# Kernel tuning notes

Hardware: AMD Instinct MI355X
Metric: run time of the kernel (lower is better)

## Reference

```python
import jax, jax.numpy as jnp
import numpy as np

B, S, D, H = 2, 2048, 1024, 16
HD = D // H  # head dim = 64


def setup_inputs() -> dict:
    key = jax.random.key(0)
    ks = jax.random.split(key, 5)
    scale = 1.0 / np.sqrt(D)
    return {
        "hidden_states": jax.random.normal(ks[0], (B, S, D), jnp.float32),
        "attention_mask": jax.random.normal(ks[1], (B, 1, 1, S), jnp.float32),
        "Wq": jax.random.normal(ks[2], (D, D), jnp.float32) * scale,
        "bq": jnp.zeros((D,), jnp.float32),
        "Wk": jax.random.normal(ks[3], (D, D), jnp.float32) * scale,
        "bk": jnp.zeros((D,), jnp.float32),
        "Wv": jax.random.normal(ks[4], (D, D), jnp.float32) * scale,
        "bv": jnp.zeros((D,), jnp.float32),
    }


def _split_heads(x):
    # [B,S,D] -> [B,H,S,HD]
    return x.reshape(B, S, H, HD).transpose(0, 2, 1, 3)


def reference(hidden_states, attention_mask, Wq, bq, Wk, bk, Wv, bv):
    # torch Linear: y = x @ W.T + b
    q = _split_heads(hidden_states @ Wq.T + bq)
    k = _split_heads(hidden_states @ Wk.T + bk)
    v = _split_heads(hidden_states @ Wv.T + bv)

    scores = jnp.einsum("bhqd,bhkd->bhqk", q, k)
    # Faithful to source: with a mask present, the 1/sqrt(head_dim) scaling
    # is overwritten and raw scores are multiplied by the binary key mask.
    mask = (attention_mask >= 0).astype(scores.dtype)  # [B,1,1,S]
    probs = scores * mask
    # dropout prob = 0 (eval) -> identity

    ctx = jnp.einsum("bhqk,bhkd->bhqd", probs, v)
    ctx = ctx.transpose(0, 2, 1, 3).reshape(B, S, D)
    return ctx
```

## Files before the change

### kernel.cpp

```cpp
#include <hip/hip_runtime.h>

#define BB 2
#define SS 2048
#define DD 1024
#define HH 16
#define HDIM 64
#define MTOT 4096

typedef unsigned short u16;
typedef __bf16 bf16_t;
typedef bf16_t bf16x8 __attribute__((ext_vector_type(8)));
typedef float floatx4 __attribute__((ext_vector_type(4)));
typedef float floatx16 __attribute__((ext_vector_type(16)));

__device__ __forceinline__ float bf2f(u16 u) {
  union { unsigned int i; float f; } x;
  x.i = ((unsigned int)u) << 16;
  return x.f;
}
__device__ __forceinline__ u16 f2bf(float f) {
  union { float f; unsigned int i; } x;
  x.f = f;
  unsigned int r = x.i + 0x7fffu + ((x.i >> 16) & 1u);
  return (u16)(r >> 16);
}

__device__ __forceinline__ void gload16(const u16* g, u16* l) {
  __builtin_amdgcn_global_load_lds(
      (const __attribute__((address_space(1))) unsigned int*)g,
      (__attribute__((address_space(3))) unsigned int*)l, 16, 0, 0);
}

__global__ __launch_bounds__(256) void cast_panel(
    const float* __restrict__ hs, const float* __restrict__ wq,
    const float* __restrict__ wk, const float* __restrict__ wv,
    u16* __restrict__ hs_p, u16* __restrict__ wq_p,
    u16* __restrict__ wk_p, u16* __restrict__ wv_p) {
  __shared__ u16 sT[64 * 72];
  const int bx = blockIdx.x, y = blockIdx.y;
  const float* src; u16* dst; int r0, R;
  if (bx < 64) { src = hs; dst = hs_p; r0 = bx * 64; R = 4096; }
  else {
    int w = (bx - 64) >> 4, t = (bx - 64) & 15;
    src = (w == 0) ? wq : (w == 1) ? wk : wv;
    dst = (w == 0) ? wq_p : (w == 1) ? wk_p : wv_p;
    r0 = t * 64; R = 1024;
  }
  const int c0 = y * 64;
  const int tid = threadIdx.x;
#pragma unroll
  for (int i = 0; i < 4; ++i) {
    int e = i * 256 + tid;
    int row = e >> 4, c4 = e & 15;
    float4 v = reinterpret_cast<const float4*>(src)[(size_t)(r0 + row) * 256 + (c0 >> 2) + c4];
    ushort4 o;
    o.x = f2bf(v.x); o.y = f2bf(v.y); o.z = f2bf(v.z); o.w = f2bf(v.w);
    *reinterpret_cast<ushort4*>(&sT[row * 72 + c4 * 4]) = o;
  }
  __syncthreads();
#pragma unroll
  for (int i = 0; i < 2; ++i) {
    int e = i * 256 + tid;
    int p = e >> 6, m = e & 63;
    uint4 v = *reinterpret_cast<const uint4*>(&sT[m * 72 + p * 8]);
    reinterpret_cast<uint4*>(dst)[(size_t)(y * 8 + p) * R + r0 + m] = v;
  }
}

#define BKK 32
__global__ __launch_bounds__(256) void qkv_gemm_kernel(
    const u16* __restrict__ Ap,
    const u16* __restrict__ Wqp, const u16* __restrict__ Wkp, const u16* __restrict__ Wvp,
    const float* __restrict__ bq, const float* __restrict__ bk, const float* __restrict__ bv,
    u16* __restrict__ Qo, u16* __restrict__ Ko, u16* __restrict__ Vo) {
  __shared__ u16 sA[128 * BKK];
  __shared__ u16 sB[128 * BKK];
  const int mt = blockIdx.y, ntall = blockIdx.x;
  const int seg = ntall >> 3, nt = ntall & 7;
  const u16* Wp = (seg == 0) ? Wqp : (seg == 1) ? Wkp : Wvp;
  const float* bp = (seg == 0) ? bq : (seg == 1) ? bk : bv;
  u16* Out = (seg == 0) ? Qo : (seg == 1) ? Ko : Vo;
  const int m0 = mt * 128, n0 = nt * 128;
  const int tid = threadIdx.x;
  const int lane = tid & 63, wave = tid >> 6;
  const int wm = (wave >> 1) * 64, wn = (wave & 1) * 64;
  const int l32 = lane & 31, khalf = lane >> 5;
  floatx16 acc[2][2] = {};
  for (int k0 = 0; k0 < DD; k0 += BKK) {
    const int p0 = k0 >> 3;
#pragma unroll
    for (int c = 0; c < 2; ++c) {
      const int pa = p0 + c * 2 + khalf;
      gload16(Ap + ((size_t)pa * MTOT + m0 + wave * 32 + l32) * 8,
              sA + ((wave * 2 + c) * 64 + lane) * 8);
      gload16(Wp + ((size_t)pa * 1024 + n0 + wave * 32 + l32) * 8,
              sB + ((wave * 2 + c) * 64 + lane) * 8);
    }
    __syncthreads();
#pragma unroll
    for (int kk = 0; kk < 2; ++kk) {
      bf16x8 af[2], bfr[2];
#pragma unroll
      for (int i = 0; i < 2; ++i) {
        int gA = (wave >> 1) * 2 + i;
        af[i] = *reinterpret_cast<const bf16x8*>(sA + (gA * 128 + kk * 64 + lane) * 8);
      }
#pragma unroll
      for (int j = 0; j < 2; ++j) {
        int gB = (wave & 1) * 2 + j;
        bfr[j] = *reinterpret_cast<const bf16x8*>(sB + (gB * 128 + kk * 64 + lane) * 8);
      }
#pragma unroll
      for (int i = 0; i < 2; ++i)
#pragma unroll
        for (int j = 0; j < 2; ++j)
          acc[i][j] = __builtin_amdgcn_mfma_f32_32x32x16_bf16(af[i], bfr[j], acc[i][j], 0, 0, 0);
    }
    __syncthreads();
  }
#pragma unroll
  for (int j = 0; j < 2; ++j) {
    int col = n0 + wn + j * 32 + l32;
    float bias = bp[col];
#pragma unroll
    for (int i = 0; i < 2; ++i) {
#pragma unroll
      for (int reg = 0; reg < 16; ++reg) {
        int row = m0 + wm + i * 32 + (reg & 3) + 8 * (reg >> 2) + 4 * khalf;
        Out[(size_t)row * DD + col] = f2bf(acc[i][j][reg] + bias);
      }
    }
  }
}

__global__ __launch_bounds__(256) void m_partial_kernel(
    const u16* __restrict__ Kb, const u16* __restrict__ Vb,
    const float* __restrict__ am, float* __restrict__ mpart) {
  __shared__ float sK[64 * 68];
  __shared__ float sV[64 * 68];
  const int bh = blockIdx.y;
  const int b = bh >> 4, h = bh & 15;
  const int tid = threadIdx.x;
  const int e0 = (tid & 15) * 4, d0 = (tid >> 4) * 4;
  float acc[4][4] = {};
  for (int cs = 0; cs < 4; ++cs) {
    const int s0 = (blockIdx.x * 4 + cs) * 64;
    if (cs) __syncthreads();
#pragma unroll
    for (int c = 0; c < 2; ++c) {
      int L = tid + c * 256;
      int srow = L >> 3;
      int col = (L & 7) * 8;
      size_t g = (size_t)(b * SS + s0 + srow) * DD + h * HDIM + col;
      uint4 kraw = *reinterpret_cast<const uint4*>(Kb + g);
      uint4 vraw = *reinterpret_cast<const uint4*>(Vb + g);
      float m = (am[b * SS + s0 + srow] >= 0.f) ? 1.f : 0.f;
      unsigned int kw[4] = {kraw.x, kraw.y, kraw.z, kraw.w};
      unsigned int vw[4] = {vraw.x, vraw.y, vraw.z, vraw.w};
#pragma unroll
      for (int q = 0; q < 4; ++q) {
        sK[srow * 68 + col + 2 * q]     = m * bf2f((u16)(kw[q] & 0xffffu));
        sK[srow * 68 + col + 2 * q + 1] = m * bf2f((u16)(kw[q] >> 16));
        sV[srow * 68 + col + 2 * q]     = bf2f((u16)(vw[q] & 0xffffu));
        sV[srow * 68 + col + 2 * q + 1] = bf2f((u16)(vw[q] >> 16));
      }
    }
    __syncthreads();
    for (int s = 0; s < 64; ++s) {
      float4 kk = *reinterpret_cast<const float4*>(&sK[s * 68 + e0]);
      float4 vv = *reinterpret_cast<const float4*>(&sV[s * 68 + d0]);
      float ka[4] = {kk.x, kk.y, kk.z, kk.w};
      float va[4] = {vv.x, vv.y, vv.z, vv.w};
#pragma unroll
      for (int i = 0; i < 4; ++i)
#pragma unroll
        for (int j = 0; j < 4; ++j) acc[i][j] += ka[i] * va[j];
    }
  }
  float* outp = mpart + ((size_t)(blockIdx.x * 32 + bh)) * 4096;
#pragma unroll
  for (int i = 0; i < 4; ++i) {
    float4 o = {acc[i][0], acc[i][1], acc[i][2], acc[i][3]};
    *reinterpret_cast<float4*>(&outp[(e0 + i) * 64 + d0]) = o;
  }
}

__global__ __launch_bounds__(256) void ctx_kernel(
    const u16* __restrict__ Qb, const float* __restrict__ mpart, float* __restrict__ Out) {
  __shared__ float sM[64 * 68];
  __shared__ float sQ[64 * 68];
  const int mchunk = blockIdx.x;
  const int h = blockIdx.y;
  const int m0 = mchunk * 64;
  const int b = m0 >> 11;
  const int bh = b * HH + h;
  const int tid = threadIdx.x;
#pragma unroll
  for (int c = 0; c < 4; ++c) {
    int L4 = c * 256 + tid;
    float4 s = {0.f, 0.f, 0.f, 0.f};
#pragma unroll
    for (int pc = 0; pc < 8; ++pc) {
      const float4* p4 = reinterpret_cast<const float4*>(mpart + ((size_t)(pc * 32 + bh)) * 4096);
      float4 t = p4[L4];
      s.x += t.x; s.y += t.y; s.z += t.z; s.w += t.w;
    }
    int e = L4 >> 4, d = (L4 & 15) * 4;
    *reinterpret_cast<float4*>(&sM[e * 68 + d]) = s;
  }
#pragma unroll
  for (int c = 0; c < 2; ++c) {
    int L = tid + c * 256;
    int row = L >> 3, col = (L & 7) * 8;
    uint4 q = *reinterpret_cast<const uint4*>(Qb + (size_t)(m0 + row) * DD + h * HDIM + col);
    unsigned int w[4] = {q.x, q.y, q.z, q.w};
#pragma unroll
    for (int t = 0; t < 4; ++t) {
      sQ[row * 68 + col + 2 * t]     = bf2f((u16)(w[t] & 0xffffu));
      sQ[row * 68 + col + 2 * t + 1] = bf2f((u16)(w[t] >> 16));
    }
  }
  __syncthreads();
  const int d0 = (tid & 15) * 4, ml0 = (tid >> 4) * 4;
  float acc[4][4] = {};
  for (int e4 = 0; e4 < 64; e4 += 4) {
    float4 mm[4], qq[4];
#pragma unroll
    for (int t = 0; t < 4; ++t)
      mm[t] = *reinterpret_cast<const float4*>(&sM[(e4 + t) * 68 + d0]);
#pragma unroll
    for (int i = 0; i < 4; ++i)
      qq[i] = *reinterpret_cast<const float4*>(&sQ[(ml0 + i) * 68 + e4]);
    float ma[4][4], qa[4][4];
#pragma unroll
    for (int t = 0; t < 4; ++t) {
      ma[t][0] = mm[t].x; ma[t][1] = mm[t].y; ma[t][2] = mm[t].z; ma[t][3] = mm[t].w;
      qa[t][0] = qq[t].x; qa[t][1] = qq[t].y; qa[t][2] = qq[t].z; qa[t][3] = qq[t].w;
    }
#pragma unroll
    for (int i = 0; i < 4; ++i)
#pragma unroll
      for (int t = 0; t < 4; ++t)
#pragma unroll
        for (int j = 0; j < 4; ++j)
          acc[i][j] += qa[i][t] * ma[t][j];
  }
#pragma unroll
  for (int i = 0; i < 4; ++i) {
    float4 o = {acc[i][0], acc[i][1], acc[i][2], acc[i][3]};
    *reinterpret_cast<float4*>(Out + (size_t)(m0 + ml0 + i) * DD + h * HDIM + d0) = o;
  }
}

extern "C" void kernel_launch(void* const* d_in, const int* in_sizes, int n_in,
                              void* d_out, int out_size, void* d_ws, size_t ws_size,
                              hipStream_t stream) {
  const float* hs = (const float*)d_in[0];
  const float* am = (const float*)d_in[1];
  const float* wq = (const float*)d_in[2];
  const float* bq = (const float*)d_in[3];
  const float* wk = (const float*)d_in[4];
  const float* bk = (const float*)d_in[5];
  const float* wv = (const float*)d_in[6];
  const float* bv = (const float*)d_in[7];
  float* out = (float*)d_out;
  char* ws = (char*)d_ws;

  u16* hs_p = (u16*)(ws);
  u16* wq_p = (u16*)(ws + 8388608);
  u16* wk_p = (u16*)(ws + 10485760);
  u16* wv_p = (u16*)(ws + 12582912);
  u16* q_b  = (u16*)(ws + 14680064);
  u16* k_b  = (u16*)(ws + 23068672);
  u16* v_b  = (u16*)(ws + 31457280);
  float* mpart = (float*)(ws + 39845888);

  cast_panel<<<dim3(112, 16), 256, 0, stream>>>(hs, wq, wk, wv, hs_p, wq_p, wk_p, wv_p);
  qkv_gemm_kernel<<<dim3(24, 32), 256, 0, stream>>>(hs_p, wq_p, wk_p, wv_p,
                                                    bq, bk, bv, q_b, k_b, v_b);
  m_partial_kernel<<<dim3(8, 32), 256, 0, stream>>>(k_b, v_b, am, mpart);
  ctx_kernel<<<dim3(64, 16), 256, 0, stream>>>(q_b, mpart, out);
}
```

Measured before the change: 161.7 us.

## Load GEMM fragments directly from global into registers with double buffering

The QKV projection GEMM no longer stages A and W panels through LDS with global_load_lds and barriers. Each wave now reads its MFMA fragments straight from the pre-packed global layout into registers, using a two-stage register ping-pong so the next k-step's loads are in flight while the current MFMAs run. This removes LDS traffic and both __syncthreads per k-step. In exchange, each wave re-reads data that neighbouring waves in the block also use, which raises global/L2 traffic, and it needs more registers.

```diff
diff --git a/kernel.cpp b/kernel.cpp
--- a/kernel.cpp
+++ b/kernel.cpp
@@ -23,12 +23,6 @@
   x.f = f;
   unsigned int r = x.i + 0x7fffu + ((x.i >> 16) & 1u);
   return (u16)(r >> 16);
-}
-
-__device__ __forceinline__ void gload16(const u16* g, u16* l) {
-  __builtin_amdgcn_global_load_lds(
-      (const __attribute__((address_space(1))) unsigned int*)g,
-      (__attribute__((address_space(3))) unsigned int*)l, 16, 0, 0);
 }
 
 __global__ __launch_bounds__(256) void cast_panel(
@@ -67,15 +61,12 @@
   }
 }
 
-#define BKK 32
 __global__ __launch_bounds__(256) void qkv_gemm_kernel(
     const u16* __restrict__ Ap,
     const u16* __restrict__ Wqp, const u16* __restrict__ Wkp, const u16* __restrict__ Wvp,
     const float* __restrict__ bq, const float* __restrict__ bk, const float* __restrict__ bv,
     u16* __restrict__ Qo, u16* __restrict__ Ko, u16* __restrict__ Vo) {
-  __shared__ u16 sA[128 * BKK];
-  __shared__ u16 sB[128 * BKK];
-  const int mt = blockIdx.y, ntall = blockIdx.x;
+  const int ntall = blockIdx.x, mt = blockIdx.y;
   const int seg = ntall >> 3, nt = ntall & 7;
   const u16* Wp = (seg == 0) ? Wqp : (seg == 1) ? Wkp : Wvp;
   const float* bp = (seg == 0) ? bq : (seg == 1) ? bk : bv;
@@ -85,38 +76,40 @@
   const int lane = tid & 63, wave = tid >> 6;
   const int wm = (wave >> 1) * 64, wn = (wave & 1) * 64;
   const int l32 = lane & 31, khalf = lane >> 5;
+  const u16* apb = Ap + ((size_t)khalf * MTOT + m0 + wm + l32) * 8;
+  const u16* bpb = Wp + ((size_t)khalf * 1024 + n0 + wn + l32) * 8;
+  const size_t aStep = (size_t)4 * MTOT * 8;
+  const size_t bStep = (size_t)4 * 1024 * 8;
   floatx16 acc[2][2] = {};
-  for (int k0 = 0; k0 < DD; k0 += BKK) {
-    const int p0 = k0 >> 3;
-#pragma unroll
-    for (int c = 0; c < 2; ++c) {
-      const int pa = p0 + c * 2 + khalf;
-      gload16(Ap + ((size_t)pa * MTOT + m0 + wave * 32 + l32) * 8,
-              sA + ((wave * 2 + c) * 64 + lane) * 8);
-      gload16(Wp + ((size_t)pa * 1024 + n0 + wave * 32 + l32) * 8,
-              sB + ((wave * 2 + c) * 64 + lane) * 8);
-    }
-    __syncthreads();
-#pragma unroll
-    for (int kk = 0; kk < 2; ++kk) {
-      bf16x8 af[2], bfr[2];
+
+  auto loadfr = [&](bf16x8 (&a)[2][2], bf16x8 (&b)[2][2], int s) {
+    const u16* ap = apb + (size_t)s * aStep;
+    const u16* bp2 = bpb + (size_t)s * bStep;
+#pragma unroll
+    for (int kk = 0; kk < 2; ++kk)
 #pragma unroll
       for (int i = 0; i < 2; ++i) {
-        int gA = (wave >> 1) * 2 + i;
-        af[i] = *reinterpret_cast<const bf16x8*>(sA + (gA * 128 + kk * 64 + lane) * 8);
+        a[kk][i] = *reinterpret_cast<const bf16x8*>(ap + ((size_t)kk * 2 * MTOT + i * 32) * 8);
+        b[kk][i] = *reinterpret_cast<const bf16x8*>(bp2 + ((size_t)kk * 2 * 1024 + i * 32) * 8);
       }
-#pragma unroll
-      for (int j = 0; j < 2; ++j) {
-        int gB = (wave & 1) * 2 + j;
-        bfr[j] = *reinterpret_cast<const bf16x8*>(sB + (gB * 128 + kk * 64 + lane) * 8);
-      }
+  };
+  auto mfmall = [&](bf16x8 (&a)[2][2], bf16x8 (&b)[2][2]) {
+#pragma unroll
+    for (int kk = 0; kk < 2; ++kk)
 #pragma unroll
       for (int i = 0; i < 2; ++i)
 #pragma unroll
         for (int j = 0; j < 2; ++j)
-          acc[i][j] = __builtin_amdgcn_mfma_f32_32x32x16_bf16(af[i], bfr[j], acc[i][j], 0, 0, 0);
-    }
-    __syncthreads();
+          acc[i][j] = __builtin_amdgcn_mfma_f32_32x32x16_bf16(a[kk][i], b[kk][j], acc[i][j], 0, 0, 0);
+  };
+
+  bf16x8 aC[2][2], bC[2][2], aN[2][2], bN[2][2];
+  loadfr(aC, bC, 0);
+  for (int s = 0; s < 32; s += 2) {
+    loadfr(aN, bN, s + 1);
+    mfmall(aC, bC);
+    if (s + 2 < 32) loadfr(aC, bC, s + 2);
+    mfmall(aN, bN);
   }
 #pragma unroll
   for (int j = 0; j < 2; ++j) {
```

After: 162.9 us. About the same (+0.7%).
